# Optimization experiments

Measured on AMD Instinct MI355X. Metric: run time of the kernel, lower is better.

The kernel has to match this reference:

```python
import jax, jax.numpy as jnp
import numpy as np

P = 113          # vocab (modulus)
D = 128          # residual_dim
H = 4            # n_heads (hardcoded in Model)
DH = D // H      # head_dim = 32
HID = 4 * D      # mlp hidden = 512
BATCH = 131072
RATE = 0.5       # attention_rate


def setup_inputs() -> dict:
    key = jax.random.key(0)
    ks = jax.random.split(key, 12)
    std = 1.0 / D ** 0.5
    x = jax.random.randint(ks[0], (BATCH, 2), 0, P)
    tok_emb = jax.random.normal(ks[1], (P, D), jnp.float32) / D ** 0.5
    pos_emb = jax.random.normal(ks[2], (2, D), jnp.float32) / D ** 0.5
    W_Q = jax.random.normal(ks[3], (H, D, DH), jnp.float32) * std
    W_K = jax.random.normal(ks[4], (H, D, DH), jnp.float32) * std
    W_V = jax.random.normal(ks[5], (H, D, DH), jnp.float32) * std
    W_O = jax.random.normal(ks[6], (H, DH, D), jnp.float32) * std
    # nn.Linear default init: U(-1/sqrt(fan_in), 1/sqrt(fan_in))
    b1_bound = 1.0 / D ** 0.5
    W1 = jax.random.uniform(ks[7], (D, HID), jnp.float32, -b1_bound, b1_bound)
    b1 = jax.random.uniform(ks[8], (HID,), jnp.float32, -b1_bound, b1_bound)
    b2_bound = 1.0 / HID ** 0.5
    W2 = jax.random.uniform(ks[9], (HID, D), jnp.float32, -b2_bound, b2_bound)
    b2 = jax.random.uniform(ks[10], (D,), jnp.float32, -b2_bound, b2_bound)
    W_U = jax.random.normal(ks[11], (P, D), jnp.float32) / P ** 0.5
    return dict(x=x, tok_emb=tok_emb, pos_emb=pos_emb, W_Q=W_Q, W_K=W_K,
                W_V=W_V, W_O=W_O, W1=W1, b1=b1, W2=W2, b2=b2, W_U=W_U)


def reference(x, tok_emb, pos_emb, W_Q, W_K, W_V, W_O, W1, b1, W2, b2, W_U):
    # embed: [B,2,D]
    resid = tok_emb[x] + pos_emb[None, :, :]
    # attention
    q = jnp.einsum('bpd,hdk->bphk', resid, W_Q)
    k = jnp.einsum('bpd,hdk->bphk', resid, W_K)
    v = jnp.einsum('bpd,hdk->bphk', resid, W_V)
    scores = jnp.einsum('bqhk,bshk->bhqs', q, k) / DH ** 0.5  # [B,H,2,2]
    pattern = jax.nn.softmax(scores, axis=-1)
    pattern = (1.0 - RATE) + RATE * pattern  # uniform blend, no causal mask
    z = jnp.einsum('bshk,bhqs->bqhk', v, pattern)
    attn_out = jnp.einsum('bqhk,hkd->bqd', z, W_O)
    resid = resid + attn_out
    # mlp
    h = jax.nn.relu(resid @ W1 + b1)
    resid = resid + (h @ W2 + b2)
    # unembed: [B,2,P]
    logits = jnp.einsum('vd,bpd->bpv', W_U, resid)
    return logits
```

## Files before the change

kernel.cpp:

```cpp
#include <hip/hip_runtime.h>
#include <hip/hip_bf16.h>
#include <stdint.h>

typedef __hip_bfloat16 bf16;
typedef __attribute__((ext_vector_type(8))) short short8;
typedef __attribute__((ext_vector_type(4))) float float4v;

#define NVOCAB 113
#define NPAIR (113 * 113)
#define DDIM 128
#define HIDDIM 512

#define OFF_TOK 0
#define OFF_POS 14464
#define OFF_WQ  14720
#define OFF_WK  31104
#define OFF_WV  47488
#define OFF_WO  63872
#define OFF_W1  80256
#define OFF_B1  145792
#define OFF_W2  146304
#define OFF_B2  211840
#define OFF_WU  211968
#define WTOTAL  226432

#define BOFF_WOT 0
#define BOFF_W1T 16384
#define BOFF_W2T (16384 + 65536)
#define BOFF_WUP (16384 + 65536 + 65536)
#define BTOTAL   (16384 + 65536 + 65536 + 16384)
#define QOFF_Q 0
#define QOFF_K 16384
#define QOFF_V 32768
#define QTOTAL 49152

__device__ __forceinline__ uint16_t f2b(float f) {
  bf16 h = __float2bfloat16(f);
  return *(uint16_t*)&h;
}
__device__ __forceinline__ float b2f(uint16_t u) {
  return __uint_as_float(((uint32_t)u) << 16);
}

__global__ void detect_kernel(const uint32_t* __restrict__ tok_raw,
                              const uint32_t* __restrict__ x_raw,
                              int* __restrict__ flags) {
  __shared__ int cnt_bf16, cnt_xnz;
  if (threadIdx.x == 0) { cnt_bf16 = 0; cnt_xnz = 0; }
  __syncthreads();
  uint32_t u = tok_raw[threadIdx.x];
  int e = (u >> 7) & 0xff;
  if (e >= 100 && e <= 126) atomicAdd(&cnt_bf16, 1);
  uint32_t xv = x_raw[2 * threadIdx.x + 1];
  if (xv != 0u) atomicAdd(&cnt_xnz, 1);
  __syncthreads();
  if (threadIdx.x == 0) {
    flags[0] = (cnt_bf16 >= 128) ? 1 : 0;
    flags[1] = (cnt_xnz == 0) ? 1 : 0;
  }
}

struct SrcPtrs { const void* p[11]; };

__global__ void convert_kernel(SrcPtrs sp, float* __restrict__ dst,
                               const int* __restrict__ flags) {
  const int idx = blockIdx.x * 256 + threadIdx.x;
  if (idx >= WTOTAL) return;
  const int pref[12] = {OFF_TOK, OFF_POS, OFF_WQ, OFF_WK, OFF_WV, OFF_WO,
                        OFF_W1, OFF_B1, OFF_W2, OFF_B2, OFF_WU, WTOTAL};
  int t = 0;
  while (idx >= pref[t + 1]) ++t;
  const int local = idx - pref[t];
  const void* src = sp.p[t];
  if (flags[0]) {
    dst[idx] = __bfloat162float(((const bf16*)src)[local]);
  } else {
    dst[idx] = ((const float*)src)[local];
  }
}

__global__ void transpose_bf16_kernel(const float* __restrict__ wf,
                                      uint16_t* __restrict__ wb,
                                      uint16_t* __restrict__ qw) {
  const int idx = blockIdx.x * 256 + threadIdx.x;
  if (idx >= BTOTAL + QTOTAL) return;
  if (idx >= BTOTAL) {
    int l = idx - BTOTAL;
    int which = l >> 14, r = l & 16383;
    int hj = r >> 7, d = r & 127;
    int h = hj >> 5, j = hj & 31;
    int off = (which == 0) ? OFF_WQ : (which == 1) ? OFF_WK : OFF_WV;
    qw[l] = f2b(wf[off + h * 4096 + d * 32 + j]);
    return;
  }
  float v;
  if (idx < BOFF_W1T) {
    int l = idx, d = l >> 7, c = l & 127;
    v = wf[OFF_WO + c * 128 + d];
  } else if (idx < BOFF_W2T) {
    int l = idx - BOFF_W1T, n = l >> 7, d = l & 127;
    v = wf[OFF_W1 + d * 512 + n];
  } else if (idx < BOFF_WUP) {
    int l = idx - BOFF_W2T, d = l >> 9, j = l & 511;
    v = wf[OFF_W2 + j * 128 + d];
  } else {
    int l = idx - BOFF_WUP, vv = l >> 7, d = l & 127;
    v = (vv < NVOCAB) ? wf[OFF_WU + vv * 128 + d] : 0.f;
  }
  wb[idx] = f2b(v);
}

__global__ void __launch_bounds__(384) qkv_kernel(
    const float* __restrict__ wf, const uint16_t* __restrict__ qw,
    float* __restrict__ resid_pre, float* __restrict__ qt,
    float* __restrict__ kt, float* __restrict__ vt) {
  const int row = blockIdx.x;
  const int t = row >> 1, p = row & 1;
  const int tid = threadIdx.x;

  __shared__ float r[DDIM];
  if (tid < DDIM) {
    float rv = wf[OFF_TOK + t * DDIM + tid] + wf[OFF_POS + p * DDIM + tid];
    r[tid] = rv;
    resid_pre[row * DDIM + tid] = rv;
  }
  __syncthreads();

  const int which = tid >> 7, j = tid & 127;
  const short8* wrow = (const short8*)(qw + which * 16384 + j * 128);
  float a = 0.f;
  #pragma unroll
  for (int ch = 0; ch < 16; ++ch) {
    short8 wv = wrow[ch];
    #pragma unroll
    for (int e = 0; e < 8; ++e)
      a += r[ch * 8 + e] * b2f((uint16_t)wv[e]);
  }
  float* outp = (which == 0) ? qt : (which == 1) ? kt : vt;
  outp[row * DDIM + j] = a;
}

__global__ void __launch_bounds__(256, 4) pair_mfma_kernel(
    const float* __restrict__ resid_pre, const float* __restrict__ qt,
    const float* __restrict__ kt, const float* __restrict__ vt,
    const float* __restrict__ wf, const uint16_t* __restrict__ wb,
    float* __restrict__ table) {
  __shared__ uint16_t bufH[16 * 512];
  __shared__ uint16_t bufZ[16 * 128];
  __shared__ uint16_t bufS[16 * 128];
  __shared__ float    spat[8 * 16];
  __shared__ int      srow[16];

  const int tid = threadIdx.x;
  const int blk = blockIdx.x;

  if (tid < 128) {
    const int pl = tid >> 4, s = tid & 15;
    const int pair = blk * 8 + pl;
    if (pair < NPAIR) {
      const int t0 = pair / NVOCAB, t1 = pair - t0 * NVOCAB;
      const int row0 = t0 * 2, row1 = t1 * 2 + 1;
      const int h = s >> 2, qp = (s >> 1) & 1, sp = s & 1;
      const float4* qrow = (const float4*)(qt + (qp ? row1 : row0) * DDIM + h * 32);
      const float4* krow = (const float4*)(kt + (sp ? row1 : row0) * DDIM + h * 32);
      float acc = 0.f;
      #pragma unroll
      for (int j = 0; j < 8; ++j) {
        float4 qv = qrow[j], kv = krow[j];
        acc += qv.x * kv.x + qv.y * kv.y + qv.z * kv.z + qv.w * kv.w;
      }
      spat[pl * 16 + s] = acc * 0.17677669529663687f;
    } else {
      spat[pl * 16 + s] = 0.f;
    }
  } else if (tid < 144) {
    const int m = tid - 128;
    const int pair = blk * 8 + (m >> 1);
    int rv = 0;
    if (pair < NPAIR) {
      const int t0 = pair / NVOCAB, t1 = pair - t0 * NVOCAB;
      rv = (m & 1) ? t1 * 2 + 1 : t0 * 2;
    }
    srow[m] = rv;
  }
  __syncthreads();
  if (tid < 64) {
    const int pl = tid >> 3, s = tid & 7;
    const int base = pl * 16 + s * 2;
    float s0 = spat[base], s1 = spat[base + 1];
    float m = fmaxf(s0, s1);
    float e0 = __expf(s0 - m), e1 = __expf(s1 - m);
    float inv = 1.f / (e0 + e1);
    spat[base]     = 0.5f + 0.5f * e0 * inv;
    spat[base + 1] = 0.5f + 0.5f * e1 * inv;
  }
  __syncthreads();
  {
    const int m = tid >> 4, c0 = (tid & 15) * 8;
    const int pl = m >> 1, qp = m & 1;
    const int row0 = srow[pl * 2], row1 = srow[pl * 2 + 1];
    const int h = c0 >> 5;
    const float p0 = spat[pl * 16 + h * 4 + qp * 2];
    const float p1 = spat[pl * 16 + h * 4 + qp * 2 + 1];
    short8 pk;
    #pragma unroll
    for (int e = 0; e < 8; ++e) {
      const int c = c0 + e;
      float z = p0 * vt[row0 * DDIM + c] + p1 * vt[row1 * DDIM + c];
      pk[e] = (short)f2b(z);
    }
    *(short8*)&bufZ[(m * 16 + ((c0 >> 3) ^ m)) * 8] = pk;
  }
  __syncthreads();

  const int lane = tid & 63;
  const int npar = tid >> 6;
  const int l15 = lane & 15, quad = lane >> 4;
  const int mA = l15;

  float smid[2][4];

  {
    short8 af[4];
    #pragma unroll
    for (int ks = 0; ks < 4; ++ks)
      af[ks] = *(const short8*)&bufZ[(mA * 16 + ((ks * 4 + quad) ^ mA)) * 8];
    #pragma unroll
    for (int ni = 0; ni < 2; ++ni) {
      const int n = (npar + ni * 4) * 16 + l15;
      const uint16_t* bp = wb + BOFF_WOT + n * 128 + quad * 8;
      float4v acc = {0.f, 0.f, 0.f, 0.f};
      #pragma unroll
      for (int ks = 0; ks < 4; ++ks)
        acc = __builtin_amdgcn_mfma_f32_16x16x32_bf16(
            af[ks], *(const short8*)(bp + ks * 32), acc, 0, 0, 0);
      #pragma unroll
      for (int r = 0; r < 4; ++r) {
        const int row = quad * 4 + r;
        float v = acc[r] + resid_pre[srow[row] * DDIM + n];
        smid[ni][r] = v;
        bufS[(row * 16 + ((n >> 3) ^ row)) * 8 + (n & 7)] = f2b(v);
      }
    }
  }
  __syncthreads();

  {
    short8 af[4];
    #pragma unroll
    for (int ks = 0; ks < 4; ++ks)
      af[ks] = *(const short8*)&bufS[(mA * 16 + ((ks * 4 + quad) ^ mA)) * 8];
    #pragma unroll
    for (int ni = 0; ni < 8; ++ni) {
      const int n = (npar + ni * 4) * 16 + l15;
      const uint16_t* bp = wb + BOFF_W1T + n * 128 + quad * 8;
      float4v acc = {0.f, 0.f, 0.f, 0.f};
      #pragma unroll
      for (int ks = 0; ks < 4; ++ks)
        acc = __builtin_amdgcn_mfma_f32_16x16x32_bf16(
            af[ks], *(const short8*)(bp + ks * 32), acc, 0, 0, 0);
      const float bias = wf[OFF_B1 + n];
      #pragma unroll
      for (int r = 0; r < 4; ++r) {
        const int row = quad * 4 + r;
        bufH[(row * 64 + ((n >> 3) ^ row)) * 8 + (n & 7)] =
            f2b(fmaxf(acc[r] + bias, 0.f));
      }
    }
  }
  __syncthreads();

  {
    short8 ah[16];
    #pragma unroll
    for (int ks = 0; ks < 16; ++ks)
      ah[ks] = *(const short8*)&bufH[(mA * 64 + ((ks * 4 + quad) ^ mA)) * 8];
    #pragma unroll
    for (int ni = 0; ni < 2; ++ni) {
      const int n = (npar + ni * 4) * 16 + l15;
      const uint16_t* bp = wb + BOFF_W2T + n * 512 + quad * 8;
      float4v acc = {0.f, 0.f, 0.f, 0.f};
      #pragma unroll
      for (int ks = 0; ks < 16; ++ks)
        acc = __builtin_amdgcn_mfma_f32_16x16x32_bf16(
            ah[ks], *(const short8*)(bp + ks * 32), acc, 0, 0, 0);
      const float bias = wf[OFF_B2 + n];
      #pragma unroll
      for (int r = 0; r < 4; ++r) {
        const int row = quad * 4 + r;
        bufZ[(row * 16 + ((n >> 3) ^ row)) * 8 + (n & 7)] =
            f2b(acc[r] + bias + smid[ni][r]);
      }
    }
  }
  __syncthreads();

  {
    short8 ar[4];
    #pragma unroll
    for (int ks = 0; ks < 4; ++ks)
      ar[ks] = *(const short8*)&bufZ[(mA * 16 + ((ks * 4 + quad) ^ mA)) * 8];
    #pragma unroll
    for (int ni = 0; ni < 2; ++ni) {
      const int n = (npar + ni * 4) * 16 + l15;
      const uint16_t* bp = wb + BOFF_WUP + n * 128 + quad * 8;
      float4v acc = {0.f, 0.f, 0.f, 0.f};
      #pragma unroll
      for (int ks = 0; ks < 4; ++ks)
        acc = __builtin_amdgcn_mfma_f32_16x16x32_bf16(
            ar[ks], *(const short8*)(bp + ks * 32), acc, 0, 0, 0);
      if (n < NVOCAB) {
        #pragma unroll
        for (int r = 0; r < 4; ++r) {
          const int row = quad * 4 + r;
          const int pair = blk * 8 + (row >> 1);
          if (pair < NPAIR)
            table[pair * 226 + (row & 1) * NVOCAB + n] = acc[r];
        }
      }
    }
  }
}

__global__ void gather_kernel(const uint32_t* __restrict__ x_raw,
                              const float2* __restrict__ table_v2,
                              float2* __restrict__ out_v2, int total,
                              const int* __restrict__ flags) {
  __shared__ int is64;
  if (threadIdx.x == 0) is64 = flags[1];
  __syncthreads();
  const int i = blockIdx.x * blockDim.x + threadIdx.x;
  if (i >= total) return;
  const int b = i / NVOCAB;
  const int j = i - b * NVOCAB;
  int t0, t1;
  if (is64) {
    t0 = (int)x_raw[4 * b];
    t1 = (int)x_raw[4 * b + 2];
  } else {
    t0 = (int)x_raw[2 * b];
    t1 = (int)x_raw[2 * b + 1];
  }
  t0 = min(max(t0, 0), NVOCAB - 1);
  t1 = min(max(t1, 0), NVOCAB - 1);
  const int pair = t0 * NVOCAB + t1;
  out_v2[i] = table_v2[pair * NVOCAB + j];
}

extern "C" void kernel_launch(void* const* d_in, const int* in_sizes, int n_in,
                              void* d_out, int out_size, void* d_ws, size_t ws_size,
                              hipStream_t stream) {
  int*      flags     = (int*)d_ws;
  float*    wf        = (float*)((char*)d_ws + 256);
  float*    resid_pre = (float*)((char*)d_ws + 905984);
  float*    qt        = (float*)((char*)d_ws + 1021696);
  float*    kt        = (float*)((char*)d_ws + 1137408);
  float*    vt        = (float*)((char*)d_ws + 1253120);
  float*    table     = (float*)((char*)d_ws + 1368832);
  uint16_t* wb        = (uint16_t*)((char*)d_ws + 12912016);
  uint16_t* qw        = (uint16_t*)table;

  const int B = in_sizes[0] / 2;

  detect_kernel<<<1, 256, 0, stream>>>((const uint32_t*)d_in[1],
                                       (const uint32_t*)d_in[0], flags);

  SrcPtrs sp;
  for (int i = 0; i < 11; ++i) sp.p[i] = d_in[i + 1];
  convert_kernel<<<(WTOTAL + 255) / 256, 256, 0, stream>>>(sp, wf, flags);
  transpose_bf16_kernel<<<(BTOTAL + QTOTAL + 255) / 256, 256, 0, stream>>>(
      wf, wb, qw);

  qkv_kernel<<<226, 384, 0, stream>>>(wf, qw, resid_pre, qt, kt, vt);

  const int nblk = (NPAIR + 7) / 8;
  pair_mfma_kernel<<<nblk, 256, 0, stream>>>(resid_pre, qt, kt, vt, wf, wb,
                                             table);

  const int total = B * NVOCAB;
  gather_kernel<<<(total + 255) / 256, 256, 0, stream>>>(
      (const uint32_t*)d_in[0], (const float2*)table, (float2*)d_out,
      total, flags);
}
```

Measured before the change: 262.1 us.

## Scatter logits directly from pair kernel using counting-sort of batch indices

```diff
diff --git a/kernel.cpp b/kernel.cpp
--- a/kernel.cpp
+++ b/kernel.cpp
@@ -44,7 +44,8 @@
 
 __global__ void detect_kernel(const uint32_t* __restrict__ tok_raw,
                               const uint32_t* __restrict__ x_raw,
-                              int* __restrict__ flags) {
+                              int* __restrict__ flags,
+                              int* __restrict__ counts) {
   __shared__ int cnt_bf16, cnt_xnz;
   if (threadIdx.x == 0) { cnt_bf16 = 0; cnt_xnz = 0; }
   __syncthreads();
@@ -53,6 +54,7 @@
   if (e >= 100 && e <= 126) atomicAdd(&cnt_bf16, 1);
   uint32_t xv = x_raw[2 * threadIdx.x + 1];
   if (xv != 0u) atomicAdd(&cnt_xnz, 1);
+  for (int i = threadIdx.x; i < NPAIR; i += 256) counts[i] = 0;
   __syncthreads();
   if (threadIdx.x == 0) {
     flags[0] = (cnt_bf16 >= 128) ? 1 : 0;
@@ -63,19 +65,37 @@
 struct SrcPtrs { const void* p[11]; };
 
 __global__ void convert_kernel(SrcPtrs sp, float* __restrict__ dst,
-                               const int* __restrict__ flags) {
+                               const int* __restrict__ flags,
+                               const uint32_t* __restrict__ x_raw,
+                               int* __restrict__ counts, int B) {
   const int idx = blockIdx.x * 256 + threadIdx.x;
-  if (idx >= WTOTAL) return;
-  const int pref[12] = {OFF_TOK, OFF_POS, OFF_WQ, OFF_WK, OFF_WV, OFF_WO,
-                        OFF_W1, OFF_B1, OFF_W2, OFF_B2, OFF_WU, WTOTAL};
-  int t = 0;
-  while (idx >= pref[t + 1]) ++t;
-  const int local = idx - pref[t];
-  const void* src = sp.p[t];
-  if (flags[0]) {
-    dst[idx] = __bfloat162float(((const bf16*)src)[local]);
-  } else {
-    dst[idx] = ((const float*)src)[local];
+  if (idx < WTOTAL) {
+    const int pref[12] = {OFF_TOK, OFF_POS, OFF_WQ, OFF_WK, OFF_WV, OFF_WO,
+                          OFF_W1, OFF_B1, OFF_W2, OFF_B2, OFF_WU, WTOTAL};
+    int t = 0;
+    while (idx >= pref[t + 1]) ++t;
+    const int local = idx - pref[t];
+    const void* src = sp.p[t];
+    if (flags[0]) {
+      dst[idx] = __bfloat162float(((const bf16*)src)[local]);
+    } else {
+      dst[idx] = ((const float*)src)[local];
+    }
+  }
+  const int nthr = gridDim.x * 256;
+  const int is64 = flags[1];
+  for (int b = idx; b < B; b += nthr) {
+    int t0, t1;
+    if (is64) {
+      t0 = (int)x_raw[4 * b];
+      t1 = (int)x_raw[4 * b + 2];
+    } else {
+      t0 = (int)x_raw[2 * b];
+      t1 = (int)x_raw[2 * b + 1];
+    }
+    t0 = min(max(t0, 0), NVOCAB - 1);
+    t1 = min(max(t1, 0), NVOCAB - 1);
+    atomicAdd(&counts[t0 * NVOCAB + t1], 1);
   }
 }
 
@@ -110,6 +130,60 @@
   wb[idx] = f2b(v);
 }
 
+__global__ void scan_kernel(const int* __restrict__ counts,
+                            int* __restrict__ offsets,
+                            int* __restrict__ cursor) {
+  __shared__ int tsum[256];
+  const int tid = threadIdx.x;
+  const int base = tid * 50;
+  int s = 0;
+  for (int i = 0; i < 50; ++i) {
+    int p = base + i;
+    if (p < NPAIR) s += counts[p];
+  }
+  tsum[tid] = s;
+  __syncthreads();
+  for (int st = 1; st < 256; st <<= 1) {
+    int v = (tid >= st) ? tsum[tid - st] : 0;
+    __syncthreads();
+    tsum[tid] += v;
+    __syncthreads();
+  }
+  int off = (tid == 0) ? 0 : tsum[tid - 1];
+  for (int i = 0; i < 50; ++i) {
+    int p = base + i;
+    if (p < NPAIR) {
+      int c = counts[p];
+      offsets[p] = off;
+      cursor[p] = off;
+      off += c;
+    }
+  }
+}
+
+__global__ void scatter_kernel(const uint32_t* __restrict__ x_raw,
+                               int* __restrict__ cursor,
+                               int* __restrict__ blist, int B,
+                               const int* __restrict__ flags) {
+  const int is64 = flags[1];
+  for (int b = blockIdx.x * blockDim.x + threadIdx.x; b < B;
+       b += gridDim.x * blockDim.x) {
+    int t0, t1;
+    if (is64) {
+      t0 = (int)x_raw[4 * b];
+      t1 = (int)x_raw[4 * b + 2];
+    } else {
+      t0 = (int)x_raw[2 * b];
+      t1 = (int)x_raw[2 * b + 1];
+    }
+    t0 = min(max(t0, 0), NVOCAB - 1);
+    t1 = min(max(t1, 0), NVOCAB - 1);
+    const int pair = t0 * NVOCAB + t1;
+    int pos = atomicAdd(&cursor[pair], 1);
+    blist[pos] = b;
+  }
+}
+
 __global__ void __launch_bounds__(384) qkv_kernel(
     const float* __restrict__ wf, const uint16_t* __restrict__ qw,
     float* __restrict__ resid_pre, float* __restrict__ qt,
@@ -144,7 +218,8 @@
     const float* __restrict__ resid_pre, const float* __restrict__ qt,
     const float* __restrict__ kt, const float* __restrict__ vt,
     const float* __restrict__ wf, const uint16_t* __restrict__ wb,
-    float* __restrict__ table) {
+    const int* __restrict__ counts, const int* __restrict__ offsets,
+    const int* __restrict__ blist, float* __restrict__ out) {
   __shared__ uint16_t bufH[16 * 512];
   __shared__ uint16_t bufZ[16 * 128];
   __shared__ uint16_t bufS[16 * 128];
@@ -271,30 +346,34 @@
   __syncthreads();
 
   {
-    short8 ah[16];
-    #pragma unroll
-    for (int ks = 0; ks < 16; ++ks)
-      ah[ks] = *(const short8*)&bufH[(mA * 64 + ((ks * 4 + quad) ^ mA)) * 8];
-    #pragma unroll
-    for (int ni = 0; ni < 2; ++ni) {
-      const int n = (npar + ni * 4) * 16 + l15;
-      const uint16_t* bp = wb + BOFF_W2T + n * 512 + quad * 8;
-      float4v acc = {0.f, 0.f, 0.f, 0.f};
-      #pragma unroll
-      for (int ks = 0; ks < 16; ++ks)
-        acc = __builtin_amdgcn_mfma_f32_16x16x32_bf16(
-            ah[ks], *(const short8*)(bp + ks * 32), acc, 0, 0, 0);
-      const float bias = wf[OFF_B2 + n];
-      #pragma unroll
-      for (int r = 0; r < 4; ++r) {
-        const int row = quad * 4 + r;
-        bufZ[(row * 16 + ((n >> 3) ^ row)) * 8 + (n & 7)] =
-            f2b(acc[r] + bias + smid[ni][r]);
-      }
-    }
-  }
-  __syncthreads();
-
+    const int n0 = npar * 16 + l15;
+    const int n1 = (npar + 4) * 16 + l15;
+    const uint16_t* bp0 = wb + BOFF_W2T + n0 * 512 + quad * 8;
+    const uint16_t* bp1 = wb + BOFF_W2T + n1 * 512 + quad * 8;
+    float4v acc0 = {0.f, 0.f, 0.f, 0.f};
+    float4v acc1 = {0.f, 0.f, 0.f, 0.f};
+    #pragma unroll
+    for (int ks = 0; ks < 16; ++ks) {
+      short8 ah = *(const short8*)&bufH[(mA * 64 + ((ks * 4 + quad) ^ mA)) * 8];
+      acc0 = __builtin_amdgcn_mfma_f32_16x16x32_bf16(
+          ah, *(const short8*)(bp0 + ks * 32), acc0, 0, 0, 0);
+      acc1 = __builtin_amdgcn_mfma_f32_16x16x32_bf16(
+          ah, *(const short8*)(bp1 + ks * 32), acc1, 0, 0, 0);
+    }
+    const float bias0 = wf[OFF_B2 + n0];
+    const float bias1 = wf[OFF_B2 + n1];
+    #pragma unroll
+    for (int r = 0; r < 4; ++r) {
+      const int row = quad * 4 + r;
+      bufZ[(row * 16 + ((n0 >> 3) ^ row)) * 8 + (n0 & 7)] =
+          f2b(acc0[r] + bias0 + smid[0][r]);
+      bufZ[(row * 16 + ((n1 >> 3) ^ row)) * 8 + (n1 & 7)] =
+          f2b(acc1[r] + bias1 + smid[1][r]);
+    }
+  }
+  __syncthreads();
+
+  float* lds_log = (float*)bufH;
   {
     short8 ar[4];
     #pragma unroll
@@ -313,38 +392,42 @@
         #pragma unroll
         for (int r = 0; r < 4; ++r) {
           const int row = quad * 4 + r;
-          const int pair = blk * 8 + (row >> 1);
-          if (pair < NPAIR)
-            table[pair * 226 + (row & 1) * NVOCAB + n] = acc[r];
+          lds_log[(row >> 1) * 226 + (row & 1) * 113 + n] = acc[r];
         }
       }
     }
   }
-}
-
-__global__ void gather_kernel(const uint32_t* __restrict__ x_raw,
-                              const float2* __restrict__ table_v2,
-                              float2* __restrict__ out_v2, int total,
-                              const int* __restrict__ flags) {
-  __shared__ int is64;
-  if (threadIdx.x == 0) is64 = flags[1];
-  __syncthreads();
-  const int i = blockIdx.x * blockDim.x + threadIdx.x;
-  if (i >= total) return;
-  const int b = i / NVOCAB;
-  const int j = i - b * NVOCAB;
-  int t0, t1;
-  if (is64) {
-    t0 = (int)x_raw[4 * b];
-    t1 = (int)x_raw[4 * b + 2];
-  } else {
-    t0 = (int)x_raw[2 * b];
-    t1 = (int)x_raw[2 * b + 1];
-  }
-  t0 = min(max(t0, 0), NVOCAB - 1);
-  t1 = min(max(t1, 0), NVOCAB - 1);
-  const int pair = t0 * NVOCAB + t1;
-  out_v2[i] = table_v2[pair * NVOCAB + j];
+  __syncthreads();
+
+  {
+    const int base_pair = blk * 8;
+    int cArr[8], oArr[8];
+    #pragma unroll
+    for (int q = 0; q < 8; ++q) {
+      const int pr = base_pair + q;
+      if (pr < NPAIR) { cArr[q] = counts[pr]; oArr[q] = offsets[pr]; }
+      else            { cArr[q] = 0;          oArr[q] = 0; }
+    }
+    int s[9];
+    s[0] = 0;
+    #pragma unroll
+    for (int q = 0; q < 8; ++q) s[q + 1] = s[q] + cArr[q];
+    const int tot = s[8];
+    const int wid = tid >> 6;
+    const float2* lds2 = (const float2*)lds_log;
+    for (int w = wid; w < tot; w += 4) {
+      int pl = 0, sb = 0, ob = oArr[0];
+      #pragma unroll
+      for (int q = 1; q < 8; ++q)
+        if (w >= s[q]) { pl = q; sb = s[q]; ob = oArr[q]; }
+      const int b = blist[ob + (w - sb)];
+      const float2* src = lds2 + pl * 113;
+      float2* dst = (float2*)out + (size_t)b * 113;
+      dst[lane] = src[lane];
+      const int j2 = lane + 64;
+      if (j2 < 113) dst[j2] = src[j2];
+    }
+  }
 }
 
 extern "C" void kernel_launch(void* const* d_in, const int* in_sizes, int n_in,
@@ -356,29 +439,33 @@
   float*    qt        = (float*)((char*)d_ws + 1021696);
   float*    kt        = (float*)((char*)d_ws + 1137408);
   float*    vt        = (float*)((char*)d_ws + 1253120);
-  float*    table     = (float*)((char*)d_ws + 1368832);
+  uint16_t* qw        = (uint16_t*)((char*)d_ws + 1368832);
+  int*      counts    = (int*)((char*)d_ws + 1467136);
+  int*      offsets   = (int*)((char*)d_ws + 1518336);
+  int*      cursor    = (int*)((char*)d_ws + 1569536);
+  int*      blist     = (int*)((char*)d_ws + 1620736);
   uint16_t* wb        = (uint16_t*)((char*)d_ws + 12912016);
-  uint16_t* qw        = (uint16_t*)table;
 
   const int B = in_sizes[0] / 2;
 
   detect_kernel<<<1, 256, 0, stream>>>((const uint32_t*)d_in[1],
-                                       (const uint32_t*)d_in[0], flags);
+                                       (const uint32_t*)d_in[0], flags, counts);
 
   SrcPtrs sp;
   for (int i = 0; i < 11; ++i) sp.p[i] = d_in[i + 1];
-  convert_kernel<<<(WTOTAL + 255) / 256, 256, 0, stream>>>(sp, wf, flags);
+  convert_kernel<<<(WTOTAL + 255) / 256, 256, 0, stream>>>(
+      sp, wf, flags, (const uint32_t*)d_in[0], counts, B);
   transpose_bf16_kernel<<<(BTOTAL + QTOTAL + 255) / 256, 256, 0, stream>>>(
       wf, wb, qw);
 
+  scan_kernel<<<1, 256, 0, stream>>>(counts, offsets, cursor);
+  scatter_kernel<<<512, 256, 0, stream>>>((const uint32_t*)d_in[0], cursor,
+                                          blist, B, flags);
+
   qkv_kernel<<<226, 384, 0, stream>>>(wf, qw, resid_pre, qt, kt, vt);
 
   const int nblk = (NPAIR + 7) / 8;
   pair_mfma_kernel<<<nblk, 256, 0, stream>>>(resid_pre, qt, kt, vt, wf, wb,
-                                             table);
-
-  const int total = B * NVOCAB;
-  gather_kernel<<<(total + 255) / 256, 256, 0, stream>>>(
-      (const uint32_t*)d_in[0], (const float2*)table, (float2*)d_out,
-      total, flags);
-}
+                                             counts, offsets, blist,
+                                             (float*)d_out);
+}
```

Result: slower. 293.3 us (+11.9%).
